# Kernel tuning notes

Measured on AMD Instinct MI355X. Metric: run time of the kernel, lower is better.

## Reference

```python
import jax, jax.numpy as jnp
import numpy as np

B, S, D, E = 8, 2048, 1024, 8
TOKENS = B * S
CAPACITY = TOKENS // E  # capacity_factor=1.0, top-1 gating (deepspeed default)


def _moe_layer(x_flat, Wg, We, be):
    """DeepSpeed-style top-1 MoE: gate -> capacity drop -> dispatch -> expert GEMM -> combine.
    x_flat: [T, D]; Wg: [D, E]; We: [E, D, D]; be: [E, D]."""
    gates = jax.nn.softmax(x_flat @ Wg, axis=-1)              # [T, E]
    idx = jnp.argmax(gates, axis=1)                            # [T] expert per token
    mask = jax.nn.one_hot(idx, E, dtype=jnp.int32)             # [T, E]
    loc = jnp.cumsum(mask, axis=0) - 1                         # position within expert
    loc_s = jnp.sum(loc * mask, axis=1)                        # [T]
    keep = loc_s < CAPACITY                                    # capacity drop
    gate_s = jnp.sum(gates * mask.astype(gates.dtype), axis=1) * keep.astype(gates.dtype)
    slot = jnp.clip(loc_s, 0, CAPACITY - 1)
    # dispatch: scatter kept tokens into [E, C, D] buffer (slots are unique for kept tokens)
    disp = jnp.zeros((E, CAPACITY, D), x_flat.dtype).at[idx, slot].add(
        x_flat * keep[:, None].astype(x_flat.dtype))
    # grouped expert GEMM
    eo = jnp.einsum('ecd,edf->ecf', disp, We) + be[:, None, :]  # [E, C, D]
    # combine: gather each token's expert output, scale by its gate value
    return eo[idx, slot] * gate_s[:, None]                      # [T, D]


def reference(x, y, W1, b1, Wg2, We2, be2, Wg3, We3, be3):
    h = jnp.einsum('bsd,df->bsf', x, W1) + b1                  # dense pre-layer
    hf = h.reshape(TOKENS, D)
    o = _moe_layer(hf, Wg2, We2, be2)
    o = _moe_layer(o, Wg3, We3, be3)
    h = h + o.reshape(B, S, D)                                 # residual add
    sent = h.mean(axis=1)                                      # [B, D]
    logp = jax.nn.log_softmax(sent, axis=-1)
    return -jnp.mean(logp[jnp.arange(B), y])                   # CrossEntropyLoss


def setup_inputs() -> dict:
    key = jax.random.key(0)
    ks = jax.random.split(key, 10)
    s = 0.02
    return {
        'x': jax.random.normal(ks[0], (B, S, D), jnp.float32),
        'y': jax.random.randint(ks[1], (B,), 0, D),
        'W1': jax.random.normal(ks[2], (D, D), jnp.float32) * s,
        'b1': jnp.zeros((D,), jnp.float32),
        'Wg2': jax.random.normal(ks[3], (D, E), jnp.float32) * s,
        'We2': jax.random.normal(ks[4], (E, D, D), jnp.float32) * s,
        'be2': jnp.zeros((E, D), jnp.float32),
        'Wg3': jax.random.normal(ks[5], (D, E), jnp.float32) * s,
        'We3': jax.random.normal(ks[6], (E, D, D), jnp.float32) * s,
        'be3': jnp.zeros((E, D), jnp.float32),
    }
```

## Files before the change

kernel.cpp:

```cpp
#include <hip/hip_runtime.h>
#include <hip/hip_bf16.h>
#include <math.h>


#define TOKS 16384
#define DIM 1024
#define NEXP 8
#define CAP 2048
#define BATCH 8
#define SEQ 2048

typedef __bf16 bf16_t;
typedef __bf16 bf16x8 __attribute__((ext_vector_type(8)));
typedef float fx4 __attribute__((ext_vector_type(4)));

__device__ __forceinline__ void gll16(const bf16_t* g, bf16_t* l) {
  __builtin_amdgcn_global_load_lds(
      (const __attribute__((address_space(1))) unsigned int*)g,
      (__attribute__((address_space(3))) unsigned int*)l, 16, 0, 0);
}

__global__ __launch_bounds__(256) void k_prep_w(
    const float* __restrict__ W1, const float* __restrict__ We2,
    const float* __restrict__ We3, bf16_t* __restrict__ Wt) {
  __shared__ float t[64][65];
  const int m = blockIdx.z;
  const float* src = (m == 0) ? W1
                     : (m <= 8) ? We2 + (size_t)(m - 1) * DIM * DIM
                                : We3 + (size_t)(m - 9) * DIM * DIM;
  bf16_t* dst = Wt + (size_t)m * DIM * DIM;
  const int n0 = blockIdx.x * 64, k0 = blockIdx.y * 64;
  const int tid = threadIdx.x;
  const int r = tid >> 4, c4 = (tid & 15) * 4;
#pragma unroll
  for (int i = 0; i < 4; i++) {
    float4 v = *(const float4*)&src[(size_t)(k0 + i * 16 + r) * DIM + n0 + c4];
    t[i * 16 + r][c4] = v.x;
    t[i * 16 + r][c4 + 1] = v.y;
    t[i * 16 + r][c4 + 2] = v.z;
    t[i * 16 + r][c4 + 3] = v.w;
  }
  __syncthreads();
#pragma unroll
  for (int i = 0; i < 4; i++) {
    int rn = i * 16 + r;
    union { bf16_t b[4]; uint2 u; } tmp;
#pragma unroll
    for (int j = 0; j < 4; j++) tmp.b[j] = (bf16_t)t[c4 + j][rn];
    *(uint2*)&dst[(size_t)(n0 + rn) * DIM + k0 + c4] = tmp.u;
  }
}

__global__ __launch_bounds__(256) void k_prep_wg(
    const float* __restrict__ Wg2, const float* __restrict__ Wg3,
    bf16_t* __restrict__ WgP) {
  const int which = blockIdx.x;
  const float* src = which ? Wg3 : Wg2;
  bf16_t* dst = WgP + which * (128 * 8 * 8);
  const int tid = threadIdx.x;
#pragma unroll
  for (int j = 0; j < 4; j++) {
    int d = tid * 4 + j;
    float4 a = *(const float4*)&src[d * 8];
    float4 b = *(const float4*)&src[d * 8 + 4];
    float v[8] = {a.x, a.y, a.z, a.w, b.x, b.y, b.z, b.w};
#pragma unroll
    for (int e = 0; e < 8; e++)
      dst[((d >> 3) * 8 + e) * 8 + (d & 7)] = (bf16_t)v[e];
  }
}

__global__ __launch_bounds__(256) void k_cvt_x(const float* __restrict__ x,
                                               bf16_t* __restrict__ xb) {
  size_t i = ((size_t)blockIdx.x * 256 + threadIdx.x) * 8;
  float4 a = *(const float4*)&x[i];
  float4 b = *(const float4*)&x[i + 4];
  union { bf16_t h[8]; uint4 u; } t;
  t.h[0] = (bf16_t)a.x; t.h[1] = (bf16_t)a.y; t.h[2] = (bf16_t)a.z; t.h[3] = (bf16_t)a.w;
  t.h[4] = (bf16_t)b.x; t.h[5] = (bf16_t)b.y; t.h[6] = (bf16_t)b.z; t.h[7] = (bf16_t)b.w;
  *(uint4*)&xb[i] = t.u;
}

__global__ __launch_bounds__(256) void k_gemm_dense(
    const bf16_t* __restrict__ A, const bf16_t* __restrict__ Bt,
    const float* __restrict__ bias, bf16_t* __restrict__ out) {
  __shared__ alignas(16) bf16_t As[128 * 64];
  __shared__ alignas(16) bf16_t Bs[128 * 64];
  const int tid = threadIdx.x;
  const int lane = tid & 63, wave = tid >> 6;
  const int quad = lane >> 4, l15 = lane & 15;
  const int wr = (wave >> 1) * 64, wc = (wave & 1) * 64;
  const int id = blockIdx.x;
  const int j_ = id >> 3;
  const int m0 = ((id & 7) * 16 + (j_ >> 3)) * 128;
  const int n0 = (j_ & 7) * 128;
  const int kc = (tid & 7) ^ ((tid >> 3) & 7);
  const int rbase = tid >> 3;

  const bf16_t* gA[4];
  const bf16_t* gB[4];
  bf16_t* lA[4];
  bf16_t* lB[4];
#pragma unroll
  for (int i = 0; i < 4; i++) {
    int r = rbase + 32 * i;
    gA[i] = A + (size_t)(m0 + r) * DIM + kc * 8;
    gB[i] = Bt + (size_t)(n0 + r) * DIM + kc * 8;
    lA[i] = &As[(wave * 64 + 256 * i) * 8];
    lB[i] = &Bs[(wave * 64 + 256 * i) * 8];
  }

  fx4 acc[4][4];
#pragma unroll
  for (int i = 0; i < 4; i++)
#pragma unroll
    for (int j = 0; j < 4; j++) acc[i][j] = (fx4)0.0f;

  for (int k0 = 0; k0 < DIM; k0 += 64) {
#pragma unroll
    for (int i = 0; i < 4; i++) gll16(gA[i] + k0, lA[i]);
#pragma unroll
    for (int i = 0; i < 4; i++) gll16(gB[i] + k0, lB[i]);
    __syncthreads();
#pragma unroll
    for (int s = 0; s < 2; s++) {
      const int pofs = ((s * 4 + quad) ^ (l15 & 7)) << 3;
      bf16x8 av[4], bv[4];
#pragma unroll
      for (int i = 0; i < 4; i++)
        av[i] = *(const bf16x8*)&As[(wr + i * 16 + l15) * 64 + pofs];
#pragma unroll
      for (int j = 0; j < 4; j++)
        bv[j] = *(const bf16x8*)&Bs[(wc + j * 16 + l15) * 64 + pofs];
#pragma unroll
      for (int i = 0; i < 4; i++)
#pragma unroll
        for (int j = 0; j < 4; j++)
          acc[i][j] = __builtin_amdgcn_mfma_f32_16x16x32_bf16(av[i], bv[j], acc[i][j], 0, 0, 0);
    }
    __syncthreads();
  }
#pragma unroll
  for (int j = 0; j < 4; j++) {
    int col = n0 + wc + j * 16 + l15;
    float bb = bias[col];
#pragma unroll
    for (int i = 0; i < 4; i++)
#pragma unroll
      for (int r = 0; r < 4; r++) {
        int m = m0 + wr + i * 16 + quad * 4 + r;
        out[(size_t)m * DIM + col] = (bf16_t)(acc[i][j][r] + bb);
      }
  }
}

__global__ __launch_bounds__(256) void k_gate_mm(
    const bf16_t* __restrict__ act, const bf16_t* __restrict__ WgP,
    int* __restrict__ idx, float* __restrict__ gate) {
  __shared__ alignas(16) bf16_t As[64 * 64];
  __shared__ alignas(16) bf16_t WgS[128 * 64];
  __shared__ float L[64][8];
  const int tid = threadIdx.x;
  const int lane = tid & 63, wave = tid >> 6;
  const int quad = lane >> 4, l15 = lane & 15;
  const int m0 = blockIdx.x * 64;
  const int kc = (tid & 7) ^ ((tid >> 3) & 7);
  const int rbase = tid >> 3;

#pragma unroll
  for (int j = 0; j < 4; j++)
    gll16(WgP + (j * 256 + wave * 64 + lane) * 8,
          &WgS[(j * 256 + wave * 64) * 8]);

  const bf16_t* gA[2];
  bf16_t* lA[2];
#pragma unroll
  for (int i = 0; i < 2; i++) {
    gA[i] = act + (size_t)(m0 + rbase + 32 * i) * DIM + kc * 8;
    lA[i] = &As[wave * 512 + i * 2048];
  }

  fx4 acc = (fx4)0.0f;
  for (int k0 = 0; k0 < DIM; k0 += 64) {
#pragma unroll
    for (int i = 0; i < 2; i++) gll16(gA[i] + k0, lA[i]);
    __syncthreads();
#pragma unroll
    for (int s = 0; s < 2; s++) {
      const int pofs = ((s * 4 + quad) ^ (l15 & 7)) << 3;
      bf16x8 av = *(const bf16x8*)&As[(wave * 16 + l15) * 64 + pofs];
      bf16x8 bv = *(const bf16x8*)&WgS[((k0 >> 3) + s * 4 + quad) * 64 + (l15 & 7) * 8];
      acc = __builtin_amdgcn_mfma_f32_16x16x32_bf16(av, bv, acc, 0, 0, 0);
    }
    __syncthreads();
  }
  if (l15 < 8) {
#pragma unroll
    for (int r = 0; r < 4; r++) L[wave * 16 + quad * 4 + r][l15] = acc[r];
  }
  __syncthreads();
  if (tid < 64) {
    float lg[8];
#pragma unroll
    for (int e = 0; e < 8; e++) lg[e] = L[tid][e];
    float best = lg[0];
    int bi = 0;
#pragma unroll
    for (int e = 1; e < 8; e++)
      if (lg[e] > best) { best = lg[e]; bi = e; }
    float s = 0.f;
#pragma unroll
    for (int e = 0; e < 8; e++) s += expf(lg[e] - best);
    idx[m0 + tid] = bi;
    gate[m0 + tid] = 1.0f / s;
  }
}

__global__ __launch_bounds__(1024) void k_route(
    const int* __restrict__ idx, int* __restrict__ tok, int* __restrict__ cnt,
    int* __restrict__ drop, int* __restrict__ ndrop) {
  const int e = blockIdx.x;
  const int tid = threadIdx.x, lane = tid & 63, wv = tid >> 6;
  __shared__ int wsum[16];
  const int4* p = (const int4*)(idx + tid * 16);
  int m[16];
  int c = 0;
#pragma unroll
  for (int j = 0; j < 4; j++) {
    int4 v = p[j];
    m[j * 4 + 0] = (v.x == e);
    m[j * 4 + 1] = (v.y == e);
    m[j * 4 + 2] = (v.z == e);
    m[j * 4 + 3] = (v.w == e);
    c += m[j * 4] + m[j * 4 + 1] + m[j * 4 + 2] + m[j * 4 + 3];
  }
  int sc = c;
#pragma unroll
  for (int off = 1; off < 64; off <<= 1) {
    int n = __shfl_up(sc, off);
    if (lane >= off) sc += n;
  }
  if (lane == 63) wsum[wv] = sc;
  __syncthreads();
  int wb = 0, tot = 0;
#pragma unroll
  for (int i = 0; i < 16; i++) {
    int s = wsum[i];
    tot += s;
    if (i < wv) wb += s;
  }
  int pos = wb + sc - c;
#pragma unroll
  for (int j = 0; j < 16; j++) {
    if (m[j]) {
      if (pos < CAP) {
        tok[e * CAP + pos] = tid * 16 + j;
      } else {
        int di = atomicAdd(ndrop, 1);
        drop[di] = tid * 16 + j;
      }
      pos++;
    }
  }
  if (tid == 0) cnt[e] = tot < CAP ? tot : CAP;
}

__global__ __launch_bounds__(128) void k_zero_rows(
    bf16_t* __restrict__ buf, const int* __restrict__ drop,
    const int* __restrict__ ndrop) {
  const int nd = *ndrop;
  const uint4 z = {0u, 0u, 0u, 0u};
  for (int j = blockIdx.x; j < nd; j += gridDim.x) {
    int t = drop[j];
    ((uint4*)(buf + (size_t)t * DIM))[threadIdx.x] = z;
  }
}

__global__ __launch_bounds__(256) void k_gemm_expert(
    const bf16_t* __restrict__ Ain, const bf16_t* __restrict__ Wt,
    const float* __restrict__ be, const int* __restrict__ tok,
    const int* __restrict__ cnt, const float* __restrict__ gate,
    const bf16_t* __restrict__ zp, bf16_t* __restrict__ outp) {
  const int id = blockIdx.x;
  const int e = id & 7;
  const int j_ = id >> 3;
  const int c0 = (j_ >> 3) * 128;
  const int n0 = (j_ & 7) * 128;
  const int count = cnt[e];
  if (c0 >= count) return;
  const bf16_t* Bt = Wt + (size_t)e * DIM * DIM;
  const float* bias = be + (size_t)e * DIM;
  const int* tk = tok + e * CAP;

  __shared__ alignas(16) bf16_t As[128 * 64];
  __shared__ alignas(16) bf16_t Bs[128 * 64];
  const int tid = threadIdx.x;
  const int lane = tid & 63, wave = tid >> 6;
  const int quad = lane >> 4, l15 = lane & 15;
  const int wr = (wave >> 1) * 64, wc = (wave & 1) * 64;
  const int kc = (tid & 7) ^ ((tid >> 3) & 7);
  const int rbase = tid >> 3;

  const bf16_t* gA[4];
  const bf16_t* gB[4];
  bf16_t* lA[4];
  bf16_t* lB[4];
#pragma unroll
  for (int i = 0; i < 4; i++) {
    int r = rbase + 32 * i;
    int ca = c0 + r;
    gA[i] = (ca < count) ? Ain + (size_t)tk[ca] * DIM + kc * 8 : zp;
    gB[i] = Bt + (size_t)(n0 + r) * DIM + kc * 8;
    lA[i] = &As[(wave * 64 + 256 * i) * 8];
    lB[i] = &Bs[(wave * 64 + 256 * i) * 8];
  }

  fx4 acc[4][4];
#pragma unroll
  for (int i = 0; i < 4; i++)
#pragma unroll
    for (int j = 0; j < 4; j++) acc[i][j] = (fx4)0.0f;

  for (int k0 = 0; k0 < DIM; k0 += 64) {
#pragma unroll
    for (int i = 0; i < 4; i++) gll16(gA[i] + k0, lA[i]);
#pragma unroll
    for (int i = 0; i < 4; i++) gll16(gB[i] + k0, lB[i]);
    __syncthreads();
#pragma unroll
    for (int s = 0; s < 2; s++) {
      const int pofs = ((s * 4 + quad) ^ (l15 & 7)) << 3;
      bf16x8 av[4], bv[4];
#pragma unroll
      for (int i = 0; i < 4; i++)
        av[i] = *(const bf16x8*)&As[(wr + i * 16 + l15) * 64 + pofs];
#pragma unroll
      for (int j = 0; j < 4; j++)
        bv[j] = *(const bf16x8*)&Bs[(wc + j * 16 + l15) * 64 + pofs];
#pragma unroll
      for (int i = 0; i < 4; i++)
#pragma unroll
        for (int j = 0; j < 4; j++)
          acc[i][j] = __builtin_amdgcn_mfma_f32_16x16x32_bf16(av[i], bv[j], acc[i][j], 0, 0, 0);
    }
    __syncthreads();
  }
#pragma unroll
  for (int i = 0; i < 4; i++)
#pragma unroll
    for (int r = 0; r < 4; r++) {
      int c = c0 + wr + i * 16 + quad * 4 + r;
      if (c < count) {
        int t = tk[c];
        float g = gate[t];
#pragma unroll
        for (int j = 0; j < 4; j++) {
          int col = n0 + wc + j * 16 + l15;
          outp[(size_t)t * DIM + col] = (bf16_t)((acc[i][j][r] + bias[col]) * g);
        }
      }
    }
}

__global__ __launch_bounds__(256) void k_reduce_sent(
    const bf16_t* __restrict__ h, const bf16_t* __restrict__ o2,
    float* __restrict__ sent) {
  const int tid = threadIdx.x;
  const int d8 = (tid & 127) * 8;
  const int sg = tid >> 7;
  const int b = blockIdx.y;
  const int s0 = blockIdx.x * 64 + sg * 32;
  float acc[8] = {0.f, 0.f, 0.f, 0.f, 0.f, 0.f, 0.f, 0.f};
  const size_t base = ((size_t)b * SEQ + s0) * DIM + d8;
  for (int i = 0; i < 32; i++) {
    union { bf16_t v[8]; uint4 u; } hh, oo;
    hh.u = *(const uint4*)&h[base + (size_t)i * DIM];
    oo.u = *(const uint4*)&o2[base + (size_t)i * DIM];
#pragma unroll
    for (int j = 0; j < 8; j++) acc[j] += (float)hh.v[j] + (float)oo.v[j];
  }
#pragma unroll
  for (int j = 0; j < 8; j++)
    atomicAdd(&sent[b * DIM + d8 + j], acc[j] * (1.0f / SEQ));
}

__global__ __launch_bounds__(256) void k_loss(
    const float* __restrict__ sent, const int* __restrict__ y,
    float* __restrict__ out) {
  const int b = blockIdx.x, tid = threadIdx.x;
  const float* sb = sent + b * DIM;
  __shared__ float red[256];
  float m = -1e30f;
  for (int d = tid; d < DIM; d += 256) m = fmaxf(m, sb[d]);
  red[tid] = m;
  __syncthreads();
  for (int s = 128; s; s >>= 1) {
    if (tid < s) red[tid] = fmaxf(red[tid], red[tid + s]);
    __syncthreads();
  }
  m = red[0];
  __syncthreads();
  float sum = 0.f;
  for (int d = tid; d < DIM; d += 256) sum += expf(sb[d] - m);
  red[tid] = sum;
  __syncthreads();
  for (int s = 128; s; s >>= 1) {
    if (tid < s) red[tid] += red[tid + s];
    __syncthreads();
  }
  if (tid == 0) atomicAdd(out, (m + logf(red[0]) - sb[y[b]]) * (1.0f / BATCH));
}

extern "C" void kernel_launch(void* const* d_in, const int* in_sizes, int n_in,
                              void* d_out, int out_size, void* d_ws, size_t ws_size,
                              hipStream_t stream) {
  (void)in_sizes; (void)n_in; (void)out_size; (void)ws_size;
  const float* x   = (const float*)d_in[0];
  const int*   y   = (const int*)d_in[1];
  const float* W1  = (const float*)d_in[2];
  const float* b1  = (const float*)d_in[3];
  const float* Wg2 = (const float*)d_in[4];
  const float* We2 = (const float*)d_in[5];
  const float* be2 = (const float*)d_in[6];
  const float* Wg3 = (const float*)d_in[7];
  const float* We3 = (const float*)d_in[8];
  const float* be3 = (const float*)d_in[9];

  char* p = (char*)d_ws;
  size_t off = 0;
  auto carve = [&](size_t bytes) -> char* {
    char* r = p + off;
    off += (bytes + 255) & ~(size_t)255;
    return r;
  };
  bf16_t* Wt   = (bf16_t*)carve((size_t)17 * DIM * DIM * 2);
  bf16_t* WgP  = (bf16_t*)carve(2 * 128 * 8 * 8 * 2);
  bf16_t* h    = (bf16_t*)carve((size_t)TOKS * DIM * 2);
  bf16_t* o1   = (bf16_t*)carve((size_t)TOKS * DIM * 2);
  bf16_t* o2   = (bf16_t*)carve((size_t)TOKS * DIM * 2);
  int*    idx  = (int*)carve(TOKS * 4);
  float*  gate = (float*)carve(TOKS * 4);
  int*    tok  = (int*)carve(NEXP * CAP * 4);
  int*    cnt  = (int*)carve(NEXP * 4);
  int*    drop2 = (int*)carve(TOKS * 4);
  int*    drop3 = (int*)carve(TOKS * 4);
  size_t zoff0 = off;
  float*  sent = (float*)carve(BATCH * DIM * 4);
  bf16_t* zp   = (bf16_t*)carve(4096);
  int*    nd2  = (int*)carve(256);
  int*    nd3  = (int*)carve(256);
  size_t zbytes = off - zoff0;
  bf16_t* xb   = o2;

  hipMemsetAsync(sent, 0, zbytes, stream);
  hipMemsetAsync(d_out, 0, 4, stream);

  k_prep_w<<<dim3(16, 16, 17), 256, 0, stream>>>(W1, We2, We3, Wt);
  k_prep_wg<<<2, 256, 0, stream>>>(Wg2, Wg3, WgP);
  k_cvt_x<<<TOKS * DIM / 8 / 256, 256, 0, stream>>>(x, xb);

  k_gemm_dense<<<(TOKS / 128) * (DIM / 128), 256, 0, stream>>>(xb, Wt, b1, h);

  k_gate_mm<<<TOKS / 64, 256, 0, stream>>>(h, WgP, idx, gate);
  k_route<<<NEXP, 1024, 0, stream>>>(idx, tok, cnt, drop2, nd2);
  k_zero_rows<<<256, 128, 0, stream>>>(o1, drop2, nd2);
  k_gemm_expert<<<NEXP * (CAP / 128) * (DIM / 128), 256, 0, stream>>>(
      h, Wt + (size_t)1 * DIM * DIM, be2, tok, cnt, gate, zp, o1);

  k_gate_mm<<<TOKS / 64, 256, 0, stream>>>(o1, WgP + 128 * 8 * 8, idx, gate);
  k_route<<<NEXP, 1024, 0, stream>>>(idx, tok, cnt, drop3, nd3);
  k_zero_rows<<<256, 128, 0, stream>>>(o2, drop3, nd3);
  k_gemm_expert<<<NEXP * (CAP / 128) * (DIM / 128), 256, 0, stream>>>(
      o1, Wt + (size_t)9 * DIM * DIM, be3, tok, cnt, gate, zp, o2);

  k_reduce_sent<<<dim3(SEQ / 64, BATCH), 256, 0, stream>>>(h, o2, sent);
  k_loss<<<BATCH, 256, 0, stream>>>(sent, y, (float*)d_out);
}
```

Baseline: 398.9 us.

## Fuse prep kernels, sentence-sum into dense GEMM, drop-zeroing into routing, and loss

Merges the weight, gate-weight and input conversion kernels and the workspace memset into one launch. The dense GEMM epilogue now accumulates column sums of h into the sentence means, so the final reduction only reads o2. Dropped-token row zeroing moves into the routing kernel, and the loss computation is folded into the reduction via a last-block counter. This removes several launches and one full read of h, at the cost of float atomics in the GEMM epilogue and a serialized final block.

```diff
diff --git a/kernel.cpp b/kernel.cpp
--- a/kernel.cpp
+++ b/kernel.cpp
@@ -20,70 +20,76 @@
       (__attribute__((address_space(3))) unsigned int*)l, 16, 0, 0);
 }
 
-__global__ __launch_bounds__(256) void k_prep_w(
+#define PW_BLOCKS (17 * 256)
+#define CVT_BLOCKS (TOKS * DIM / 8 / 256)
+#define PREP_GRID (PW_BLOCKS + 2 + CVT_BLOCKS + 1)
+__global__ __launch_bounds__(256) void k_prep(
     const float* __restrict__ W1, const float* __restrict__ We2,
-    const float* __restrict__ We3, bf16_t* __restrict__ Wt) {
-  __shared__ float t[64][65];
-  const int m = blockIdx.z;
-  const float* src = (m == 0) ? W1
-                     : (m <= 8) ? We2 + (size_t)(m - 1) * DIM * DIM
-                                : We3 + (size_t)(m - 9) * DIM * DIM;
-  bf16_t* dst = Wt + (size_t)m * DIM * DIM;
-  const int n0 = blockIdx.x * 64, k0 = blockIdx.y * 64;
+    const float* __restrict__ We3, const float* __restrict__ Wg2,
+    const float* __restrict__ Wg3, const float* __restrict__ x,
+    bf16_t* __restrict__ Wt, bf16_t* __restrict__ WgP,
+    bf16_t* __restrict__ xb, uint4* __restrict__ zreg, int znq) {
+  const int id = blockIdx.x;
   const int tid = threadIdx.x;
-  const int r = tid >> 4, c4 = (tid & 15) * 4;
-#pragma unroll
-  for (int i = 0; i < 4; i++) {
-    float4 v = *(const float4*)&src[(size_t)(k0 + i * 16 + r) * DIM + n0 + c4];
-    t[i * 16 + r][c4] = v.x;
-    t[i * 16 + r][c4 + 1] = v.y;
-    t[i * 16 + r][c4 + 2] = v.z;
-    t[i * 16 + r][c4 + 3] = v.w;
-  }
-  __syncthreads();
-#pragma unroll
-  for (int i = 0; i < 4; i++) {
-    int rn = i * 16 + r;
-    union { bf16_t b[4]; uint2 u; } tmp;
-#pragma unroll
-    for (int j = 0; j < 4; j++) tmp.b[j] = (bf16_t)t[c4 + j][rn];
-    *(uint2*)&dst[(size_t)(n0 + rn) * DIM + k0 + c4] = tmp.u;
-  }
-}
-
-__global__ __launch_bounds__(256) void k_prep_wg(
-    const float* __restrict__ Wg2, const float* __restrict__ Wg3,
-    bf16_t* __restrict__ WgP) {
-  const int which = blockIdx.x;
-  const float* src = which ? Wg3 : Wg2;
-  bf16_t* dst = WgP + which * (128 * 8 * 8);
-  const int tid = threadIdx.x;
-#pragma unroll
-  for (int j = 0; j < 4; j++) {
-    int d = tid * 4 + j;
-    float4 a = *(const float4*)&src[d * 8];
-    float4 b = *(const float4*)&src[d * 8 + 4];
-    float v[8] = {a.x, a.y, a.z, a.w, b.x, b.y, b.z, b.w};
-#pragma unroll
-    for (int e = 0; e < 8; e++)
-      dst[((d >> 3) * 8 + e) * 8 + (d & 7)] = (bf16_t)v[e];
-  }
-}
-
-__global__ __launch_bounds__(256) void k_cvt_x(const float* __restrict__ x,
-                                               bf16_t* __restrict__ xb) {
-  size_t i = ((size_t)blockIdx.x * 256 + threadIdx.x) * 8;
-  float4 a = *(const float4*)&x[i];
-  float4 b = *(const float4*)&x[i + 4];
-  union { bf16_t h[8]; uint4 u; } t;
-  t.h[0] = (bf16_t)a.x; t.h[1] = (bf16_t)a.y; t.h[2] = (bf16_t)a.z; t.h[3] = (bf16_t)a.w;
-  t.h[4] = (bf16_t)b.x; t.h[5] = (bf16_t)b.y; t.h[6] = (bf16_t)b.z; t.h[7] = (bf16_t)b.w;
-  *(uint4*)&xb[i] = t.u;
+  if (id < PW_BLOCKS) {
+    __shared__ float t[64][65];
+    const int m = id >> 8, rem = id & 255;
+    const int n0 = (rem & 15) * 64, k0 = (rem >> 4) * 64;
+    const float* src = (m == 0) ? W1
+                       : (m <= 8) ? We2 + (size_t)(m - 1) * DIM * DIM
+                                  : We3 + (size_t)(m - 9) * DIM * DIM;
+    bf16_t* dst = Wt + (size_t)m * DIM * DIM;
+    const int r = tid >> 4, c4 = (tid & 15) * 4;
+#pragma unroll
+    for (int i = 0; i < 4; i++) {
+      float4 v = *(const float4*)&src[(size_t)(k0 + i * 16 + r) * DIM + n0 + c4];
+      t[i * 16 + r][c4] = v.x;
+      t[i * 16 + r][c4 + 1] = v.y;
+      t[i * 16 + r][c4 + 2] = v.z;
+      t[i * 16 + r][c4 + 3] = v.w;
+    }
+    __syncthreads();
+#pragma unroll
+    for (int i = 0; i < 4; i++) {
+      int rn = i * 16 + r;
+      union { bf16_t b[4]; uint2 u; } tmp;
+#pragma unroll
+      for (int j = 0; j < 4; j++) tmp.b[j] = (bf16_t)t[c4 + j][rn];
+      *(uint2*)&dst[(size_t)(n0 + rn) * DIM + k0 + c4] = tmp.u;
+    }
+  } else if (id < PW_BLOCKS + 2) {
+    const int which = id - PW_BLOCKS;
+    const float* src = which ? Wg3 : Wg2;
+    bf16_t* dst = WgP + which * (128 * 8 * 8);
+#pragma unroll
+    for (int j = 0; j < 4; j++) {
+      int d = tid * 4 + j;
+      float4 a = *(const float4*)&src[d * 8];
+      float4 b = *(const float4*)&src[d * 8 + 4];
+      float v[8] = {a.x, a.y, a.z, a.w, b.x, b.y, b.z, b.w};
+#pragma unroll
+      for (int e = 0; e < 8; e++)
+        dst[((d >> 3) * 8 + e) * 8 + (d & 7)] = (bf16_t)v[e];
+    }
+  } else if (id < PW_BLOCKS + 2 + CVT_BLOCKS) {
+    const int cid = id - PW_BLOCKS - 2;
+    size_t i = ((size_t)cid * 256 + tid) * 8;
+    float4 a = *(const float4*)&x[i];
+    float4 b = *(const float4*)&x[i + 4];
+    union { bf16_t h[8]; uint4 u; } t;
+    t.h[0] = (bf16_t)a.x; t.h[1] = (bf16_t)a.y; t.h[2] = (bf16_t)a.z; t.h[3] = (bf16_t)a.w;
+    t.h[4] = (bf16_t)b.x; t.h[5] = (bf16_t)b.y; t.h[6] = (bf16_t)b.z; t.h[7] = (bf16_t)b.w;
+    *(uint4*)&xb[i] = t.u;
+  } else {
+    const uint4 z = {0u, 0u, 0u, 0u};
+    for (int i = tid; i < znq; i += 256) zreg[i] = z;
+  }
 }
 
 __global__ __launch_bounds__(256) void k_gemm_dense(
     const bf16_t* __restrict__ A, const bf16_t* __restrict__ Bt,
-    const float* __restrict__ bias, bf16_t* __restrict__ out) {
+    const float* __restrict__ bias, bf16_t* __restrict__ out,
+    float* __restrict__ sent) {
   __shared__ alignas(16) bf16_t As[128 * 64];
   __shared__ alignas(16) bf16_t Bs[128 * 64];
   const int tid = threadIdx.x;
@@ -97,10 +103,7 @@
   const int kc = (tid & 7) ^ ((tid >> 3) & 7);
   const int rbase = tid >> 3;
 
-  const bf16_t* gA[4];
-  const bf16_t* gB[4];
-  bf16_t* lA[4];
-  bf16_t* lB[4];
+  const bf16_t* gA[4]; const bf16_t* gB[4]; bf16_t* lA[4]; bf16_t* lB[4];
 #pragma unroll
   for (int i = 0; i < 4; i++) {
     int r = rbase + 32 * i;
@@ -109,7 +112,6 @@
     lA[i] = &As[(wave * 64 + 256 * i) * 8];
     lB[i] = &Bs[(wave * 64 + 256 * i) * 8];
   }
-
   fx4 acc[4][4];
 #pragma unroll
   for (int i = 0; i < 4; i++)
@@ -140,22 +142,36 @@
     }
     __syncthreads();
   }
+  float bb[4], sj[4] = {0.f, 0.f, 0.f, 0.f};
+#pragma unroll
+  for (int j = 0; j < 4; j++) bb[j] = bias[n0 + wc + j * 16 + l15];
+#pragma unroll
+  for (int i = 0; i < 4; i++)
+#pragma unroll
+    for (int r = 0; r < 4; r++) {
+      int rowL = wr + i * 16 + quad * 4 + r;
+#pragma unroll
+      for (int j = 0; j < 4; j++) {
+        float v = acc[i][j][r] + bb[j];
+        sj[j] += v;
+        out[(size_t)(m0 + rowL) * DIM + n0 + wc + j * 16 + l15] = (bf16_t)v;
+      }
+    }
 #pragma unroll
   for (int j = 0; j < 4; j++) {
-    int col = n0 + wc + j * 16 + l15;
-    float bb = bias[col];
-#pragma unroll
-    for (int i = 0; i < 4; i++)
-#pragma unroll
-      for (int r = 0; r < 4; r++) {
-        int m = m0 + wr + i * 16 + quad * 4 + r;
-        out[(size_t)m * DIM + col] = (bf16_t)(acc[i][j][r] + bb);
-      }
+    sj[j] += __shfl_xor(sj[j], 16);
+    sj[j] += __shfl_xor(sj[j], 32);
+  }
+  if (quad == 0) {
+#pragma unroll
+    for (int j = 0; j < 4; j++)
+      atomicAdd(&sent[(m0 >> 11) * DIM + n0 + wc + j * 16 + l15],
+                sj[j] * (1.0f / SEQ));
   }
 }
 
 __global__ __launch_bounds__(256) void k_gate_mm(
-    const bf16_t* __restrict__ act, const bf16_t* __restrict__ WgP,
+    const bf16_t* __restrict__ act, const bf16_t* __restrict__ WgPx,
     int* __restrict__ idx, float* __restrict__ gate) {
   __shared__ alignas(16) bf16_t As[64 * 64];
   __shared__ alignas(16) bf16_t WgS[128 * 64];
@@ -169,17 +185,14 @@
 
 #pragma unroll
   for (int j = 0; j < 4; j++)
-    gll16(WgP + (j * 256 + wave * 64 + lane) * 8,
-          &WgS[(j * 256 + wave * 64) * 8]);
-
-  const bf16_t* gA[2];
-  bf16_t* lA[2];
+    gll16(WgPx + (j * 256 + wave * 64 + lane) * 8, &WgS[(j * 256 + wave * 64) * 8]);
+
+  const bf16_t* gA[2]; bf16_t* lA[2];
 #pragma unroll
   for (int i = 0; i < 2; i++) {
     gA[i] = act + (size_t)(m0 + rbase + 32 * i) * DIM + kc * 8;
     lA[i] = &As[wave * 512 + i * 2048];
   }
-
   fx4 acc = (fx4)0.0f;
   for (int k0 = 0; k0 < DIM; k0 += 64) {
 #pragma unroll
@@ -216,12 +229,14 @@
   }
 }
 
+#define DLMAX 2048
 __global__ __launch_bounds__(1024) void k_route(
     const int* __restrict__ idx, int* __restrict__ tok, int* __restrict__ cnt,
-    int* __restrict__ drop, int* __restrict__ ndrop) {
+    bf16_t* __restrict__ obuf) {
   const int e = blockIdx.x;
   const int tid = threadIdx.x, lane = tid & 63, wv = tid >> 6;
   __shared__ int wsum[16];
+  __shared__ int dlist[DLMAX];
   const int4* p = (const int4*)(idx + tid * 16);
   int m[16];
   int c = 0;
@@ -250,34 +265,34 @@
     if (i < wv) wb += s;
   }
   int pos = wb + sc - c;
+  const uint4 z = {0u, 0u, 0u, 0u};
 #pragma unroll
   for (int j = 0; j < 16; j++) {
     if (m[j]) {
+      int t = tid * 16 + j;
       if (pos < CAP) {
-        tok[e * CAP + pos] = tid * 16 + j;
+        tok[e * CAP + pos] = t;
       } else {
-        int di = atomicAdd(ndrop, 1);
-        drop[di] = tid * 16 + j;
+        int di = pos - CAP;
+        if (di < DLMAX) dlist[di] = t;
+        else
+          for (int k = 0; k < 128; k++) *(uint4*)&obuf[(size_t)t * DIM + k * 8] = z;
       }
       pos++;
     }
   }
   if (tid == 0) cnt[e] = tot < CAP ? tot : CAP;
-}
-
-__global__ __launch_bounds__(128) void k_zero_rows(
-    bf16_t* __restrict__ buf, const int* __restrict__ drop,
-    const int* __restrict__ ndrop) {
-  const int nd = *ndrop;
-  const uint4 z = {0u, 0u, 0u, 0u};
-  for (int j = blockIdx.x; j < nd; j += gridDim.x) {
-    int t = drop[j];
-    ((uint4*)(buf + (size_t)t * DIM))[threadIdx.x] = z;
+  __syncthreads();
+  int ndl = tot - CAP;
+  ndl = ndl < 0 ? 0 : (ndl > DLMAX ? DLMAX : ndl);
+  for (int d = tid >> 7; d < ndl; d += 8) {
+    int t = dlist[d];
+    *(uint4*)&obuf[(size_t)t * DIM + (tid & 127) * 8] = z;
   }
 }
 
 __global__ __launch_bounds__(256) void k_gemm_expert(
-    const bf16_t* __restrict__ Ain, const bf16_t* __restrict__ Wt,
+    const bf16_t* __restrict__ Ain, const bf16_t* __restrict__ Wt8,
     const float* __restrict__ be, const int* __restrict__ tok,
     const int* __restrict__ cnt, const float* __restrict__ gate,
     const bf16_t* __restrict__ zp, bf16_t* __restrict__ outp) {
@@ -288,7 +303,7 @@
   const int n0 = (j_ & 7) * 128;
   const int count = cnt[e];
   if (c0 >= count) return;
-  const bf16_t* Bt = Wt + (size_t)e * DIM * DIM;
+  const bf16_t* Bt = Wt8 + (size_t)e * DIM * DIM;
   const float* bias = be + (size_t)e * DIM;
   const int* tk = tok + e * CAP;
 
@@ -301,10 +316,7 @@
   const int kc = (tid & 7) ^ ((tid >> 3) & 7);
   const int rbase = tid >> 3;
 
-  const bf16_t* gA[4];
-  const bf16_t* gB[4];
-  bf16_t* lA[4];
-  bf16_t* lB[4];
+  const bf16_t* gA[4]; const bf16_t* gB[4]; bf16_t* lA[4]; bf16_t* lB[4];
 #pragma unroll
   for (int i = 0; i < 4; i++) {
     int r = rbase + 32 * i;
@@ -314,7 +326,6 @@
     lA[i] = &As[(wave * 64 + 256 * i) * 8];
     lB[i] = &Bs[(wave * 64 + 256 * i) * 8];
   }
-
   fx4 acc[4][4];
 #pragma unroll
   for (int i = 0; i < 4; i++)
@@ -345,6 +356,9 @@
     }
     __syncthreads();
   }
+  float bb[4];
+#pragma unroll
+  for (int j = 0; j < 4; j++) bb[j] = bias[n0 + wc + j * 16 + l15];
 #pragma unroll
   for (int i = 0; i < 4; i++)
 #pragma unroll
@@ -354,61 +368,71 @@
         int t = tk[c];
         float g = gate[t];
 #pragma unroll
-        for (int j = 0; j < 4; j++) {
-          int col = n0 + wc + j * 16 + l15;
-          outp[(size_t)t * DIM + col] = (bf16_t)((acc[i][j][r] + bias[col]) * g);
-        }
+        for (int j = 0; j < 4; j++)
+          outp[(size_t)t * DIM + n0 + wc + j * 16 + l15] =
+              (bf16_t)((acc[i][j][r] + bb[j]) * g);
       }
     }
 }
 
-__global__ __launch_bounds__(256) void k_reduce_sent(
-    const bf16_t* __restrict__ h, const bf16_t* __restrict__ o2,
-    float* __restrict__ sent) {
+__global__ __launch_bounds__(256) void k_reduce_loss(
+    const bf16_t* __restrict__ o2, float* __restrict__ sent,
+    const int* __restrict__ y, int* __restrict__ done,
+    float* __restrict__ out) {
   const int tid = threadIdx.x;
-  const int d8 = (tid & 127) * 8;
-  const int sg = tid >> 7;
-  const int b = blockIdx.y;
-  const int s0 = blockIdx.x * 64 + sg * 32;
-  float acc[8] = {0.f, 0.f, 0.f, 0.f, 0.f, 0.f, 0.f, 0.f};
-  const size_t base = ((size_t)b * SEQ + s0) * DIM + d8;
-  for (int i = 0; i < 32; i++) {
-    union { bf16_t v[8]; uint4 u; } hh, oo;
-    hh.u = *(const uint4*)&h[base + (size_t)i * DIM];
-    oo.u = *(const uint4*)&o2[base + (size_t)i * DIM];
-#pragma unroll
-    for (int j = 0; j < 8; j++) acc[j] += (float)hh.v[j] + (float)oo.v[j];
-  }
-#pragma unroll
-  for (int j = 0; j < 8; j++)
-    atomicAdd(&sent[b * DIM + d8 + j], acc[j] * (1.0f / SEQ));
-}
-
-__global__ __launch_bounds__(256) void k_loss(
-    const float* __restrict__ sent, const int* __restrict__ y,
-    float* __restrict__ out) {
-  const int b = blockIdx.x, tid = threadIdx.x;
-  const float* sb = sent + b * DIM;
+  {
+    const int job = blockIdx.x;
+    const int d8 = (tid & 127) * 8;
+    const int sg = tid >> 7;
+    const int b = job >> 5;
+    const int s0 = (job & 31) * 64 + sg * 32;
+    float acc[8] = {0.f, 0.f, 0.f, 0.f, 0.f, 0.f, 0.f, 0.f};
+    const size_t base = ((size_t)b * SEQ + s0) * DIM + d8;
+    for (int i = 0; i < 32; i++) {
+      union { bf16_t v[8]; uint4 u; } oo;
+      oo.u = *(const uint4*)&o2[base + (size_t)i * DIM];
+#pragma unroll
+      for (int j = 0; j < 8; j++) acc[j] += (float)oo.v[j];
+    }
+#pragma unroll
+    for (int j = 0; j < 8; j++)
+      atomicAdd(&sent[b * DIM + d8 + j], acc[j] * (1.0f / SEQ));
+  }
+  __shared__ int isLast;
+  __syncthreads();
+  if (tid == 0) {
+    __threadfence();
+    isLast = (atomicAdd(done, 1) == (int)gridDim.x - 1);
+  }
+  __syncthreads();
+  if (!isLast) return;
+  __threadfence();
   __shared__ float red[256];
-  float m = -1e30f;
-  for (int d = tid; d < DIM; d += 256) m = fmaxf(m, sb[d]);
-  red[tid] = m;
-  __syncthreads();
-  for (int s = 128; s; s >>= 1) {
-    if (tid < s) red[tid] = fmaxf(red[tid], red[tid + s]);
-    __syncthreads();
-  }
-  m = red[0];
-  __syncthreads();
-  float sum = 0.f;
-  for (int d = tid; d < DIM; d += 256) sum += expf(sb[d] - m);
-  red[tid] = sum;
-  __syncthreads();
-  for (int s = 128; s; s >>= 1) {
-    if (tid < s) red[tid] += red[tid + s];
-    __syncthreads();
-  }
-  if (tid == 0) atomicAdd(out, (m + logf(red[0]) - sb[y[b]]) * (1.0f / BATCH));
+  float total = 0.f;
+  for (int b = 0; b < BATCH; b++) {
+    const float* sb = sent + b * DIM;
+    float m = -1e30f;
+    for (int d = tid; d < DIM; d += 256) m = fmaxf(m, sb[d]);
+    red[tid] = m;
+    __syncthreads();
+    for (int s = 128; s; s >>= 1) {
+      if (tid < s) red[tid] = fmaxf(red[tid], red[tid + s]);
+      __syncthreads();
+    }
+    m = red[0];
+    __syncthreads();
+    float sum = 0.f;
+    for (int d = tid; d < DIM; d += 256) sum += expf(sb[d] - m);
+    red[tid] = sum;
+    __syncthreads();
+    for (int s = 128; s; s >>= 1) {
+      if (tid < s) red[tid] += red[tid + s];
+      __syncthreads();
+    }
+    if (tid == 0) total += m + logf(red[0]) - sb[y[b]];
+    __syncthreads();
+  }
+  if (tid == 0) out[0] = total * (1.0f / BATCH);
 }
 
 extern "C" void kernel_launch(void* const* d_in, const int* in_sizes, int n_in,
@@ -442,37 +466,29 @@
   float*  gate = (float*)carve(TOKS * 4);
   int*    tok  = (int*)carve(NEXP * CAP * 4);
   int*    cnt  = (int*)carve(NEXP * 4);
-  int*    drop2 = (int*)carve(TOKS * 4);
-  int*    drop3 = (int*)carve(TOKS * 4);
   size_t zoff0 = off;
   float*  sent = (float*)carve(BATCH * DIM * 4);
   bf16_t* zp   = (bf16_t*)carve(4096);
-  int*    nd2  = (int*)carve(256);
-  int*    nd3  = (int*)carve(256);
+  int*    done = (int*)carve(256);
   size_t zbytes = off - zoff0;
   bf16_t* xb   = o2;
 
-  hipMemsetAsync(sent, 0, zbytes, stream);
-  hipMemsetAsync(d_out, 0, 4, stream);
-
-  k_prep_w<<<dim3(16, 16, 17), 256, 0, stream>>>(W1, We2, We3, Wt);
-  k_prep_wg<<<2, 256, 0, stream>>>(Wg2, Wg3, WgP);
-  k_cvt_x<<<TOKS * DIM / 8 / 256, 256, 0, stream>>>(x, xb);
-
-  k_gemm_dense<<<(TOKS / 128) * (DIM / 128), 256, 0, stream>>>(xb, Wt, b1, h);
+  k_prep<<<PREP_GRID, 256, 0, stream>>>(
+      W1, We2, We3, Wg2, Wg3, x, Wt, WgP, xb,
+      (uint4*)sent, (int)(zbytes / 16));
+
+  k_gemm_dense<<<(TOKS / 128) * (DIM / 128), 256, 0, stream>>>(
+      xb, Wt, b1, h, sent);
 
   k_gate_mm<<<TOKS / 64, 256, 0, stream>>>(h, WgP, idx, gate);
-  k_route<<<NEXP, 1024, 0, stream>>>(idx, tok, cnt, drop2, nd2);
-  k_zero_rows<<<256, 128, 0, stream>>>(o1, drop2, nd2);
+  k_route<<<NEXP, 1024, 0, stream>>>(idx, tok, cnt, o1);
   k_gemm_expert<<<NEXP * (CAP / 128) * (DIM / 128), 256, 0, stream>>>(
       h, Wt + (size_t)1 * DIM * DIM, be2, tok, cnt, gate, zp, o1);
 
   k_gate_mm<<<TOKS / 64, 256, 0, stream>>>(o1, WgP + 128 * 8 * 8, idx, gate);
-  k_route<<<NEXP, 1024, 0, stream>>>(idx, tok, cnt, drop3, nd3);
-  k_zero_rows<<<256, 128, 0, stream>>>(o2, drop3, nd3);
+  k_route<<<NEXP, 1024, 0, stream>>>(idx, tok, cnt, o2);
   k_gemm_expert<<<NEXP * (CAP / 128) * (DIM / 128), 256, 0, stream>>>(
       o1, Wt + (size_t)9 * DIM * DIM, be3, tok, cnt, gate, zp, o2);
 
-  k_reduce_sent<<<dim3(SEQ / 64, BATCH), 256, 0, stream>>>(h, o2, sent);
-  k_loss<<<BATCH, 256, 0, stream>>>(sent, y, (float*)d_out);
-}
+  k_reduce_loss<<<256, 256, 0, stream>>>(o2, sent, y, done, (float*)d_out);
+}
```

Result: no change. 395.5 us (-0.8%).
